# Optimization experiments

Measured on AMD Instinct MI355X. Metric: run time of the kernel, lower is better.

## Reference

```python
import jax, jax.numpy as jnp
import numpy as np

# D2Q9 lattice velocities (standard ordering: rest, axis, diagonal)
E = np.array([[0,0],[1,0],[0,1],[-1,0],[0,-1],[1,1],[-1,1],[-1,-1],[1,-1]], dtype=np.int64)

# Gram-Schmidt moment matrix, row order matches the layer's eq stack:
# [rho, jx, jy, e, eps, qx, qy, pxx, pxy]
_M_np = np.array([
    [ 1,  1,  1,  1,  1,  1,  1,  1,  1],  # rho
    [ 0,  1,  0, -1,  0,  1, -1, -1,  1],  # jx
    [ 0,  0,  1,  0, -1,  1,  1, -1, -1],  # jy
    [-4, -1, -1, -1, -1,  2,  2,  2,  2],  # e
    [ 4, -2, -2, -2, -2,  1,  1,  1,  1],  # eps
    [ 0, -2,  0,  2,  0,  1, -1, -1,  1],  # qx
    [ 0,  0, -2,  0,  2,  1,  1, -1, -1],  # qy
    [ 0,  1, -1,  1, -1,  0,  0,  0,  0],  # pxx
    [ 0,  0,  0,  0,  0,  1, -1,  1, -1],  # pxy
], dtype=np.float64)
_Minv_np = np.linalg.inv(_M_np)

TAU = 0.6
GX, GY = 0.0, -1e-4
ITERATIONS = 4
NX, NY = 1024, 1024


def _stream(f):
    # periodic streaming: shift each population along its lattice velocity
    return jnp.stack(
        [jnp.roll(f[..., i], (int(E[i, 0]), int(E[i, 1])), axis=(0, 1)) for i in range(9)],
        axis=-1,
    )


def setup_inputs() -> dict:
    key = jax.random.key(0)
    kf, kw = jax.random.split(key)
    f = jax.random.uniform(kf, (NX, NY, 9), dtype=jnp.float32)
    w = jax.random.normal(kw, (7,), dtype=jnp.float32)
    return {"f": f, "w": w}


def reference(f, w):
    M = jnp.asarray(_M_np, dtype=f.dtype)
    Minv = jnp.asarray(_Minv_np, dtype=f.dtype)
    ex = jnp.asarray(E[:, 0], dtype=f.dtype)
    ey = jnp.asarray(E[:, 1], dtype=f.dtype)
    inv_tau = jnp.asarray(1.0 / TAU, dtype=f.dtype)

    for _ in range(ITERATIONS):
        # handle_boundaries: periodic (no solid nodes) -> no-op
        f = _stream(f)
        # macroscopic fields
        rho = jnp.sum(f, axis=-1)                      # [X,Y]
        vx = jnp.einsum("xyq,q->xy", f, ex) / rho
        vy = jnp.einsum("xyq,q->xy", f, ey) / rho
        # equilibrium moments with learned coefficients (gravity forcing via tau shift)
        ux = vx + TAU * GX * rho
        uy = vy + TAU * GY * rho
        jx = rho * ux
        jy = rho * uy
        j2 = jx * jx + jy * jy
        e_m = w[0] * rho + w[1] * j2
        eps = w[2] * rho - w[3] * j2
        qx = w[4] * jx
        qy = w[4] * jy
        pxx = w[5] * (jx * jx - jy * jy)
        pxy = w[6] * jx * jy
        meq = jnp.stack([rho, jx, jy, e_m, eps, qx, qy, pxx, pxy], axis=2)
        # collision in moment space, single relaxation rate 1/tau
        m = jnp.einsum("xyq,pq->xyp", f, M)
        m = m - inv_tau * (m - meq)
        f = jnp.einsum("xyp,qp->xyq", m, Minv)
    return f
```

## Files before the change

kernel.cpp:

```cpp
#include <hip/hip_runtime.h>


#define NXD 1024
#define NYD 1024
#define NCELL (NXD * NYD)
#define ROWF (NYD * 9)
#define HALF (NYD / 2)
#define HROWF (HALF * 9)

constexpr float INV_TAU = (float)(1.0 / 0.6);
constexpr float TGY     = (float)(0.6 * -1e-4);

__device__ __forceinline__ void collide1(
    float f0, float f1, float f2, float f3, float f4,
    float f5, float f6, float f7, float f8,
    const float (&w)[7],
    float& o0, float& o1, float& o2, float& o3, float& o4,
    float& o5, float& o6, float& o7, float& o8)
{
    const float rho = f0 + f1 + f2 + f3 + f4 + f5 + f6 + f7 + f8;
    const float jx0 = f1 - f3 + f5 - f6 - f7 + f8;
    const float jy0 = f2 - f4 + f5 + f6 - f7 - f8;
    const float vx = jx0 / rho;
    const float vy = jy0 / rho;
    const float uy = vy + TGY * rho;
    const float jx = rho * vx;
    const float jy = rho * uy;
    const float j2 = jx * jx + jy * jy;

    const float ax = f1 + f2 + f3 + f4;
    const float dg = f5 + f6 + f7 + f8;
    const float m3 = -4.f * f0 - ax + 2.f * dg;
    const float m4 =  4.f * f0 - 2.f * ax + dg;
    const float m5 = -2.f * f1 + 2.f * f3 + f5 - f6 - f7 + f8;
    const float m6 = -2.f * f2 + 2.f * f4 + f5 + f6 - f7 - f8;
    const float m7 = f1 - f2 + f3 - f4;
    const float m8 = f5 - f6 + f7 - f8;

    const float me3 = w[0] * rho + w[1] * j2;
    const float me4 = w[2] * rho - w[3] * j2;
    const float me5 = w[4] * jx;
    const float me6 = w[4] * jy;
    const float me7 = w[5] * (jx * jx - jy * jy);
    const float me8 = w[6] * (jx * jy);

    const float mp1 = jx0 - INV_TAU * (jx0 - jx);
    const float mp2 = jy0 - INV_TAU * (jy0 - jy);
    const float mp3 = m3  - INV_TAU * (m3 - me3);
    const float mp4 = m4  - INV_TAU * (m4 - me4);
    const float mp5 = m5  - INV_TAU * (m5 - me5);
    const float mp6 = m6  - INV_TAU * (m6 - me6);
    const float mp7 = m7  - INV_TAU * (m7 - me7);
    const float mp8 = m8  - INV_TAU * (m8 - me8);

    const float s0 = rho * (1.f / 9.f);
    const float s1 = mp1 * (1.f / 6.f);
    const float s2 = mp2 * (1.f / 6.f);
    const float s3 = mp3 * (1.f / 36.f);
    const float s4 = mp4 * (1.f / 36.f);
    const float s5 = mp5 * (1.f / 12.f);
    const float s6 = mp6 * (1.f / 12.f);
    const float s7 = mp7 * 0.25f;
    const float s8 = mp8 * 0.25f;

    const float h0 = s0 - s3 - 2.f * s4;
    const float g0 = s0 + 2.f * s3 + s4;

    o0 = s0 - 4.f * s3 + 4.f * s4;
    o1 = h0 + s1 - 2.f * s5 + s7;
    o2 = h0 + s2 - 2.f * s6 - s7;
    o3 = h0 - s1 + 2.f * s5 + s7;
    o4 = h0 - s2 + 2.f * s6 - s7;
    o5 = g0 + s1 + s2 + s5 + s6 + s8;
    o6 = g0 - s1 + s2 - s5 + s6 - s8;
    o7 = g0 - s1 - s2 - s5 - s6 + s8;
    o8 = g0 + s1 - s2 + s5 - s6 - s8;
}

__device__ __forceinline__ void collide4(const float4 (&F)[9], float4 (&O)[9],
                                         const float (&w)[7]) {
    #pragma unroll
    for (int j = 0; j < 4; ++j) {
        float f[9], o[9];
        #pragma unroll
        for (int q = 0; q < 9; ++q)
            f[q] = ((const float*)&F[q])[j];
        collide1(f[0], f[1], f[2], f[3], f[4], f[5], f[6], f[7], f[8], w,
                 o[0], o[1], o[2], o[3], o[4], o[5], o[6], o[7], o[8]);
        #pragma unroll
        for (int q = 0; q < 9; ++q)
            ((float*)&O[q])[j] = o[q];
    }
}

__device__ __forceinline__ void load_w(const float* __restrict__ wp,
                                       float (&w)[7]) {
    #pragma unroll
    for (int i = 0; i < 7; ++i) w[i] = wp[i];
}

__device__ __forceinline__ float edge_up(const float4 own,
                                         const float* __restrict__ rowp,
                                         int y0, int t) {
    float e = __shfl_up(own.w, 1, 64);
    if ((t & 63) == 0) e = rowp[(y0 - 1) & (NYD - 1)];
    return e;
}
__device__ __forceinline__ float edge_dn(const float4 own,
                                         const float* __restrict__ rowp,
                                         int y0, int t) {
    float e = __shfl_down(own.x, 1, 64);
    if ((t & 63) == 63) e = rowp[(y0 + 4) & (NYD - 1)];
    return e;
}

__device__ __forceinline__ void pull9(const float* __restrict__ src,
                                      int x, int y0, int t, float4 (&F)[9]) {
    const int xm = (x - 1) & (NXD - 1), xp = (x + 1) & (NXD - 1);
    const float* p0 = src + 0 * NCELL + x  * NYD;
    const float* p1 = src + 1 * NCELL + xm * NYD;
    const float* p2 = src + 2 * NCELL + x  * NYD;
    const float* p3 = src + 3 * NCELL + xp * NYD;
    const float* p4 = src + 4 * NCELL + x  * NYD;
    const float* p5 = src + 5 * NCELL + xm * NYD;
    const float* p6 = src + 6 * NCELL + xp * NYD;
    const float* p7 = src + 7 * NCELL + xp * NYD;
    const float* p8 = src + 8 * NCELL + xm * NYD;

    F[0] = *(const float4*)(p0 + y0);
    F[1] = *(const float4*)(p1 + y0);
    F[3] = *(const float4*)(p3 + y0);
    const float4 o2 = *(const float4*)(p2 + y0);
    const float4 o5 = *(const float4*)(p5 + y0);
    const float4 o6 = *(const float4*)(p6 + y0);
    const float4 o4 = *(const float4*)(p4 + y0);
    const float4 o7 = *(const float4*)(p7 + y0);
    const float4 o8 = *(const float4*)(p8 + y0);

    const float e2 = edge_up(o2, p2, y0, t);
    const float e5 = edge_up(o5, p5, y0, t);
    const float e6 = edge_up(o6, p6, y0, t);
    const float e4 = edge_dn(o4, p4, y0, t);
    const float e7 = edge_dn(o7, p7, y0, t);
    const float e8 = edge_dn(o8, p8, y0, t);

    F[2] = make_float4(e2, o2.x, o2.y, o2.z);
    F[5] = make_float4(e5, o5.x, o5.y, o5.z);
    F[6] = make_float4(e6, o6.x, o6.y, o6.z);
    F[4] = make_float4(o4.y, o4.z, o4.w, e4);
    F[7] = make_float4(o7.y, o7.z, o7.w, e7);
    F[8] = make_float4(o8.y, o8.z, o8.w, e8);
}

__global__ __launch_bounds__(128) void k0_t(const float* __restrict__ src,
                                            float* __restrict__ dst) {
    __shared__ float4 T[HROWF / 4];
    const int b = blockIdx.x, t = threadIdx.x;
    const int x = b >> 1, h = b & 1;

    const float4* s = (const float4*)(src + (size_t)x * ROWF + h * HROWF);
    #pragma unroll
    for (int i = 0; i < 9; ++i)
        T[t + 128 * i] = s[t + 128 * i];
    __syncthreads();

    float4 A[9];
    #pragma unroll
    for (int k = 0; k < 9; ++k) A[k] = T[t * 9 + k];
    const float* a = (const float*)A;

    const int c = x * NYD + h * HALF + 4 * t;
    #pragma unroll
    for (int q = 0; q < 9; ++q)
        *(float4*)(dst + q * NCELL + c) =
            make_float4(a[q], a[9 + q], a[18 + q], a[27 + q]);
}

__global__ __launch_bounds__(128) void k_sc(const float* __restrict__ src,
                                            float* __restrict__ dst,
                                            const float* __restrict__ wp) {
    const int b = blockIdx.x, t = threadIdx.x;
    const int x  = b >> 1;
    const int y0 = (b & 1) * HALF + 4 * t;

    float4 F[9];
    pull9(src, x, y0, t, F);

    float w[7];
    load_w(wp, w);

    float4 O[9];
    collide4(F, O, w);

    const int c = x * NYD + y0;
    #pragma unroll
    for (int q = 0; q < 9; ++q)
        *(float4*)(dst + q * NCELL + c) = O[q];
}

__global__ __launch_bounds__(128) void k4_aos(const float* __restrict__ src,
                                              float* __restrict__ dst,
                                              const float* __restrict__ wp) {
    __shared__ float4 T[HROWF / 4];
    const int b = blockIdx.x, t = threadIdx.x;
    const int x  = b >> 1;
    const int y0 = (b & 1) * HALF + 4 * t;

    float4 F[9];
    pull9(src, x, y0, t, F);

    float w[7];
    load_w(wp, w);

    float4 O[9];
    collide4(F, O, w);

    float* tt = (float*)&T[t * 9];
    #pragma unroll
    for (int f = 0; f < 36; ++f)
        tt[f] = ((const float*)&O[f % 9])[f / 9];
    __syncthreads();

    float4* dv = (float4*)(dst + (size_t)x * ROWF + (b & 1) * HROWF);
    #pragma unroll
    for (int i = 0; i < 9; ++i)
        dv[t + 128 * i] = T[t + 128 * i];
}

__global__ __launch_bounds__(256) void lbm_step_aos(const float* __restrict__ src,
                                                    float* __restrict__ dst,
                                                    const float* __restrict__ wp) {
    const int cell = blockIdx.x * 256 + threadIdx.x;
    const int x = cell >> 10;
    const int y = cell & (NYD - 1);
    const int xm = (x + NXD - 1) & (NXD - 1);
    const int xp = (x + 1) & (NXD - 1);
    const int ym = (y + NYD - 1) & (NYD - 1);
    const int yp = (y + 1) & (NYD - 1);

    const float f0 = src[(x  * NYD + y ) * 9 + 0];
    const float f1 = src[(xm * NYD + y ) * 9 + 1];
    const float f2 = src[(x  * NYD + ym) * 9 + 2];
    const float f3 = src[(xp * NYD + y ) * 9 + 3];
    const float f4 = src[(x  * NYD + yp) * 9 + 4];
    const float f5 = src[(xm * NYD + ym) * 9 + 5];
    const float f6 = src[(xp * NYD + ym) * 9 + 6];
    const float f7 = src[(xp * NYD + yp) * 9 + 7];
    const float f8 = src[(xm * NYD + yp) * 9 + 8];

    float w[7];
    load_w(wp, w);
    float o0,o1,o2,o3,o4,o5,o6,o7,o8;
    collide1(f0,f1,f2,f3,f4,f5,f6,f7,f8, w,
             o0,o1,o2,o3,o4,o5,o6,o7,o8);

    float* o = dst + (size_t)(x * NYD + y) * 9;
    o[0]=o0; o[1]=o1; o[2]=o2; o[3]=o3; o[4]=o4; o[5]=o5; o[6]=o6; o[7]=o7; o[8]=o8;
}

extern "C" void kernel_launch(void* const* d_in, const int* in_sizes, int n_in,
                              void* d_out, int out_size, void* d_ws, size_t ws_size,
                              hipStream_t stream) {
    const float* f_in = (const float*)d_in[0];
    const float* w    = (const float*)d_in[1];
    float* out = (float*)d_out;
    float* A   = (float*)d_ws;
    const size_t bufBytes = (size_t)NCELL * 9 * sizeof(float);

    dim3 grid(NXD * 2), block(128);

    if (ws_size >= 2 * bufBytes) {
        float* B = A + (size_t)NCELL * 9;
        k0_t  <<<grid, block, 0, stream>>>(f_in, A);
        k_sc  <<<grid, block, 0, stream>>>(A, B, w);
        k_sc  <<<grid, block, 0, stream>>>(B, A, w);
        k_sc  <<<grid, block, 0, stream>>>(A, B, w);
        k4_aos<<<grid, block, 0, stream>>>(B, out, w);
    } else {
        float* fin_mut = (float*)d_in[0];
        lbm_step_aos<<<4096, 256, 0, stream>>>(f_in, out, w);
        lbm_step_aos<<<4096, 256, 0, stream>>>(out, fin_mut, w);
        lbm_step_aos<<<4096, 256, 0, stream>>>(fin_mut, out, w);
        lbm_step_aos<<<4096, 256, 0, stream>>>(out, fin_mut, w);
        hipMemcpyAsync(d_out, fin_mut, bufBytes, hipMemcpyDeviceToDevice, stream);
    }
}
```

Baseline: 143.4 us.

## Fuse all LBM steps into one persistent kernel with atomic grid barriers

Replaces the five separate kernel launches with a single persistent kernel sized to resident occupancy. It performs the AoS-to-SoA transpose, four stream-collide steps and the final SoA-to-AoS write, with a software grid barrier on an atomic counter between phases. This removes the per-launch overhead and tail gaps between kernels. In exchange it adds barrier spin costs and a memset, uses 256-thread blocks that each cover a full row, and depends on every block being co-resident to avoid deadlock.

```diff
diff --git a/kernel.cpp b/kernel.cpp
--- a/kernel.cpp
+++ b/kernel.cpp
@@ -152,23 +152,116 @@
     F[8] = make_float4(o8.y, o8.z, o8.w, e8);
 }
 
+__device__ __forceinline__ void grid_barrier(int* __restrict__ bar, int step) {
+    __syncthreads();
+    if (threadIdx.x == 0) {
+        __threadfence();
+        __hip_atomic_fetch_add(bar, 1, __ATOMIC_ACQ_REL,
+                               __HIP_MEMORY_SCOPE_AGENT);
+        const int target = (int)gridDim.x * step;
+        while (__hip_atomic_load(bar, __ATOMIC_ACQUIRE,
+                                 __HIP_MEMORY_SCOPE_AGENT) < target)
+            __builtin_amdgcn_s_sleep(2);
+        __threadfence();
+    }
+    __syncthreads();
+}
+
+__global__ __launch_bounds__(256, 4) void lbm_coop(
+    const float* __restrict__ fin, float* __restrict__ out,
+    float* __restrict__ A, float* __restrict__ B,
+    const float* __restrict__ wp, int* __restrict__ bar)
+{
+    __shared__ float4 T[ROWF / 4];
+    const int t  = threadIdx.x;
+    const int nb = gridDim.x;
+
+    float w[7];
+    load_w(wp, w);
+
+    for (int x = blockIdx.x; x < NXD; x += nb) {
+        __syncthreads();
+        const float4* s = (const float4*)(fin + (size_t)x * ROWF);
+        #pragma unroll
+        for (int i = 0; i < 9; ++i)
+            T[t + 256 * i] = s[t + 256 * i];
+        __syncthreads();
+        float4 Ar[9];
+        #pragma unroll
+        for (int k = 0; k < 9; ++k) Ar[k] = T[t * 9 + k];
+        const float* a = (const float*)Ar;
+        const int c = x * NYD + 4 * t;
+        #pragma unroll
+        for (int q = 0; q < 9; ++q)
+            *(float4*)(A + q * NCELL + c) =
+                make_float4(a[q], a[9 + q], a[18 + q], a[27 + q]);
+    }
+    grid_barrier(bar, 1);
+
+    for (int x = blockIdx.x; x < NXD; x += nb) {
+        const int y0 = 4 * t;
+        float4 F[9];  pull9(A, x, y0, t, F);
+        float4 O[9];  collide4(F, O, w);
+        const int c = x * NYD + y0;
+        #pragma unroll
+        for (int q = 0; q < 9; ++q)
+            *(float4*)(B + q * NCELL + c) = O[q];
+    }
+    grid_barrier(bar, 2);
+
+    for (int x = blockIdx.x; x < NXD; x += nb) {
+        const int y0 = 4 * t;
+        float4 F[9];  pull9(B, x, y0, t, F);
+        float4 O[9];  collide4(F, O, w);
+        const int c = x * NYD + y0;
+        #pragma unroll
+        for (int q = 0; q < 9; ++q)
+            *(float4*)(A + q * NCELL + c) = O[q];
+    }
+    grid_barrier(bar, 3);
+
+    for (int x = blockIdx.x; x < NXD; x += nb) {
+        const int y0 = 4 * t;
+        float4 F[9];  pull9(A, x, y0, t, F);
+        float4 O[9];  collide4(F, O, w);
+        const int c = x * NYD + y0;
+        #pragma unroll
+        for (int q = 0; q < 9; ++q)
+            *(float4*)(B + q * NCELL + c) = O[q];
+    }
+    grid_barrier(bar, 4);
+
+    for (int x = blockIdx.x; x < NXD; x += nb) {
+        const int y0 = 4 * t;
+        float4 F[9];  pull9(B, x, y0, t, F);
+        float4 O[9];  collide4(F, O, w);
+        __syncthreads();
+        float* tt = (float*)&T[t * 9];
+        #pragma unroll
+        for (int f = 0; f < 36; ++f)
+            tt[f] = ((const float*)&O[f % 9])[f / 9];
+        __syncthreads();
+        float4* dv = (float4*)(out + (size_t)x * ROWF);
+        #pragma unroll
+        for (int i = 0; i < 9; ++i)
+            dv[t + 256 * i] = T[t + 256 * i];
+    }
+}
+
 __global__ __launch_bounds__(128) void k0_t(const float* __restrict__ src,
                                             float* __restrict__ dst) {
     __shared__ float4 T[HROWF / 4];
     const int b = blockIdx.x, t = threadIdx.x;
     const int x = b >> 1, h = b & 1;
-
     const float4* s = (const float4*)(src + (size_t)x * ROWF + h * HROWF);
     #pragma unroll
     for (int i = 0; i < 9; ++i)
         T[t + 128 * i] = s[t + 128 * i];
     __syncthreads();
-
     float4 A[9];
     #pragma unroll
     for (int k = 0; k < 9; ++k) A[k] = T[t * 9 + k];
     const float* a = (const float*)A;
-
     const int c = x * NYD + h * HALF + 4 * t;
     #pragma unroll
     for (int q = 0; q < 9; ++q)
@@ -182,16 +275,9 @@
     const int b = blockIdx.x, t = threadIdx.x;
     const int x  = b >> 1;
     const int y0 = (b & 1) * HALF + 4 * t;
-
-    float4 F[9];
-    pull9(src, x, y0, t, F);
-
-    float w[7];
-    load_w(wp, w);
-
-    float4 O[9];
-    collide4(F, O, w);
-
+    float4 F[9];  pull9(src, x, y0, t, F);
+    float w[7];   load_w(wp, w);
+    float4 O[9];  collide4(F, O, w);
     const int c = x * NYD + y0;
     #pragma unroll
     for (int q = 0; q < 9; ++q)
@@ -205,22 +291,14 @@
     const int b = blockIdx.x, t = threadIdx.x;
     const int x  = b >> 1;
     const int y0 = (b & 1) * HALF + 4 * t;
-
-    float4 F[9];
-    pull9(src, x, y0, t, F);
-
-    float w[7];
-    load_w(wp, w);
-
-    float4 O[9];
-    collide4(F, O, w);
-
+    float4 F[9];  pull9(src, x, y0, t, F);
+    float w[7];   load_w(wp, w);
+    float4 O[9];  collide4(F, O, w);
     float* tt = (float*)&T[t * 9];
     #pragma unroll
     for (int f = 0; f < 36; ++f)
         tt[f] = ((const float*)&O[f % 9])[f / 9];
     __syncthreads();
-
     float4* dv = (float4*)(dst + (size_t)x * ROWF + (b & 1) * HROWF);
     #pragma unroll
     for (int i = 0; i < 9; ++i)
@@ -261,27 +339,42 @@
 extern "C" void kernel_launch(void* const* d_in, const int* in_sizes, int n_in,
                               void* d_out, int out_size, void* d_ws, size_t ws_size,
                               hipStream_t stream) {
-    const float* f_in = (const float*)d_in[0];
-    const float* w    = (const float*)d_in[1];
+    const float* fin = (const float*)d_in[0];
+    const float* wp  = (const float*)d_in[1];
     float* out = (float*)d_out;
     float* A   = (float*)d_ws;
-    const size_t bufBytes = (size_t)NCELL * 9 * sizeof(float);
-
-    dim3 grid(NXD * 2), block(128);
-
-    if (ws_size >= 2 * bufBytes) {
-        float* B = A + (size_t)NCELL * 9;
-        k0_t  <<<grid, block, 0, stream>>>(f_in, A);
-        k_sc  <<<grid, block, 0, stream>>>(A, B, w);
-        k_sc  <<<grid, block, 0, stream>>>(B, A, w);
-        k_sc  <<<grid, block, 0, stream>>>(A, B, w);
-        k4_aos<<<grid, block, 0, stream>>>(B, out, w);
+    const size_t bufFloats = (size_t)NCELL * 9;
+    const size_t bufBytes  = bufFloats * sizeof(float);
+
+    if (ws_size >= 2 * bufBytes + 256) {
+        float* B = A + bufFloats;
+        int* bar = (int*)((char*)d_ws + 2 * bufBytes);
+        hipMemsetAsync(bar, 0, 64, stream);
+
+        int perCU = 0;
+        if (hipOccupancyMaxActiveBlocksPerMultiprocessor(&perCU, lbm_coop,
+                                                         256, 0) != hipSuccess ||
+            perCU <= 0)
+            perCU = 1;
+        int nb = perCU * 256;
+        if (nb > NXD) nb = NXD;
+
+        lbm_coop<<<dim3(nb), dim3(256), 0, stream>>>(fin, out, A, B, wp, bar);
+    } else if (ws_size >= 2 * bufBytes) {
+        float* B = A + bufFloats;
+        dim3 grid(NXD * 2), block(128);
+        k0_t  <<<grid, block, 0, stream>>>(fin, A);
+        k_sc  <<<grid, block, 0, stream>>>(A, B, wp);
+        k_sc  <<<grid, block, 0, stream>>>(B, A, wp);
+        k_sc  <<<grid, block, 0, stream>>>(A, B, wp);
+        k4_aos<<<grid, block, 0, stream>>>(B, out, wp);
     } else {
         float* fin_mut = (float*)d_in[0];
-        lbm_step_aos<<<4096, 256, 0, stream>>>(f_in, out, w);
-        lbm_step_aos<<<4096, 256, 0, stream>>>(out, fin_mut, w);
-        lbm_step_aos<<<4096, 256, 0, stream>>>(fin_mut, out, w);
-        lbm_step_aos<<<4096, 256, 0, stream>>>(out, fin_mut, w);
-        hipMemcpyAsync(d_out, fin_mut, bufBytes, hipMemcpyDeviceToDevice, stream);
-    }
-}
+        lbm_step_aos<<<4096, 256, 0, stream>>>(fin, out, wp);
+        lbm_step_aos<<<4096, 256, 0, stream>>>(out, fin_mut, wp);
+        lbm_step_aos<<<4096, 256, 0, stream>>>(fin_mut, out, wp);
+        lbm_step_aos<<<4096, 256, 0, stream>>>(out, fin_mut, wp);
+        hipMemcpyAsync(d_out, fin_mut, bufBytes, hipMemcpyDeviceToDevice,
+                       stream);
+    }
+}
```

Result: slower. 461.4 us (+221.7%).
